# Performance work log

Measured on AMD Instinct MI355X. Metric: run time of the kernel, lower is better.

## Reference

```python
import jax, jax.numpy as jnp
import numpy as np

D_MODEL = 2048
N_EXPERTS = 8
LOSS_SCALE = 3e-06


def setup_inputs() -> dict:
    key = jax.random.key(0)
    k_x, k_wr, k_br, k_w, k_b = jax.random.split(key, 5)
    s = 1.0 / np.sqrt(D_MODEL)
    x = jax.random.normal(k_x, (4, 2048, D_MODEL), dtype=jnp.float32)
    # router: nn.Linear(D, E) -> weight (E, D), bias (E,)
    Wr = jax.random.uniform(k_wr, (N_EXPERTS, D_MODEL), dtype=jnp.float32, minval=-s, maxval=s)
    br = jax.random.uniform(k_br, (N_EXPERTS,), dtype=jnp.float32, minval=-s, maxval=s)
    # experts: E stacked nn.Linear(D, D) -> weight (E, D_out, D_in), bias (E, D)
    W = jax.random.uniform(k_w, (N_EXPERTS, D_MODEL, D_MODEL), dtype=jnp.float32, minval=-s, maxval=s)
    b = jax.random.uniform(k_b, (N_EXPERTS, D_MODEL), dtype=jnp.float32, minval=-s, maxval=s)
    return {"x": x, "Wr": Wr, "br": br, "W": W, "b": b}


def reference(x, Wr, br, W, b):
    B, S, D = x.shape
    E = Wr.shape[0]
    xt = x.reshape(B * S, D)          # (T, D)
    T = xt.shape[0]

    logits = xt @ Wr.T + br           # (T, E)
    probs = jax.nn.softmax(logits, axis=-1)
    idx = jnp.argmax(probs, axis=-1)  # top-1 expert per token
    topp = jnp.max(probs, axis=-1)    # gating weight
    onehot = jax.nn.one_hot(idx, E, dtype=xt.dtype)  # (T, E)

    # auxiliary load-balancing loss (matches torch compute_loss exactly)
    fractions = onehot.mean(axis=0)                              # (E,)
    probability = (onehot * topp[:, None]).sum(axis=0) / (T * T)  # (E,)
    loss = jnp.sum(fractions * probability) * LOSS_SCALE * E

    # all-expert outputs then top-1 select (dense grouped GEMM form)
    y_all = jnp.einsum('td,efd->tef', xt, W) + b[None, :, :]     # (T, E, D)
    y = jnp.einsum('tef,te->tf', y_all, onehot) * topp[:, None]  # (T, D)
    return y.reshape(B, S, D), loss
```

## Files before the change

kernel.cpp:

```cpp
#include <hip/hip_runtime.h>

typedef unsigned short u16;
typedef unsigned int u32;
typedef __attribute__((ext_vector_type(8))) __bf16 bf16x8;
typedef __attribute__((ext_vector_type(4))) float f32x4;

#define T_TOK 8192
#define DMODEL 2048
#define N_EXP 8

__device__ __forceinline__ u32 f2bf_bits(float f) {
    u32 u = __builtin_bit_cast(u32, f);
    return (u + 0x7fffu + ((u >> 16) & 1u)) >> 16;
}
__device__ __forceinline__ u32 pack2(float a, float b) {
    return f2bf_bits(a) | (f2bf_bits(b) << 16);
}

__device__ __forceinline__ void load_lds16(const u16* g, u16* l) {
    void* gnc = (void*)g;
    __builtin_amdgcn_global_load_lds(
        (__attribute__((address_space(1))) void*)gnc,
        (__attribute__((address_space(3))) void*)l,
        16, 0, 0);
}

__global__ void zero_kernel(u32* p) {
    p[threadIdx.x] = 0u;
}

__global__ void __launch_bounds__(256) convert_w_kernel(const float* __restrict__ W,
                                                        u16* __restrict__ Wb) {
    size_t i = ((size_t)blockIdx.x * 256 + threadIdx.x) * 8;
    float4 a = *(const float4*)(W + i);
    float4 b = *(const float4*)(W + i + 4);
    uint4 o;
    o.x = pack2(a.x, a.y);
    o.y = pack2(a.z, a.w);
    o.z = pack2(b.x, b.y);
    o.w = pack2(b.z, b.w);
    *(uint4*)(Wb + i) = o;
}

__global__ void __launch_bounds__(256) router_kernel(const float* __restrict__ x,
                                                     const float* __restrict__ Wr,
                                                     const float* __restrict__ br,
                                                     u16* __restrict__ xb,
                                                     int* __restrict__ perm,
                                                     float* __restrict__ topp,
                                                     int* __restrict__ counts,
                                                     float* __restrict__ sumt) {
    __shared__ int sEid[16];
    __shared__ float sTp[16];

    int tid = threadIdx.x;
    int lane = tid & 63;
    int w = tid >> 6;
    int t0 = blockIdx.x * 16 + w * 4;

    float acc[4][8];
#pragma unroll
    for (int tk = 0; tk < 4; tk++)
#pragma unroll
        for (int e = 0; e < 8; e++) acc[tk][e] = 0.0f;

#pragma unroll
    for (int i = 0; i < 8; i++) {
        int vidx = i * 64 + lane;
        float4 wv[8];
#pragma unroll
        for (int e = 0; e < 8; e++)
            wv[e] = *(const float4*)(Wr + e * DMODEL + vidx * 4);
#pragma unroll
        for (int tk = 0; tk < 4; tk++) {
            int t = t0 + tk;
            float4 xv = ((const float4*)(x + ((size_t)t << 11)))[vidx];
            uint2 pk;
            pk.x = pack2(xv.x, xv.y);
            pk.y = pack2(xv.z, xv.w);
            *(uint2*)(xb + ((size_t)t << 11) + (size_t)vidx * 4) = pk;
#pragma unroll
            for (int e = 0; e < 8; e++) {
                acc[tk][e] = fmaf(xv.x, wv[e].x, fmaf(xv.y, wv[e].y,
                              fmaf(xv.z, wv[e].z, fmaf(xv.w, wv[e].w, acc[tk][e]))));
            }
        }
    }
#pragma unroll
    for (int off = 32; off; off >>= 1)
#pragma unroll
        for (int tk = 0; tk < 4; tk++)
#pragma unroll
            for (int e = 0; e < 8; e++)
                acc[tk][e] += __shfl_xor(acc[tk][e], off, 64);

    if (lane == 0) {
#pragma unroll
        for (int tk = 0; tk < 4; tk++) {
            float lg[8];
#pragma unroll
            for (int e = 0; e < 8; e++) lg[e] = acc[tk][e] + br[e];
            float m = lg[0];
            int am = 0;
#pragma unroll
            for (int e = 1; e < 8; e++)
                if (lg[e] > m) { m = lg[e]; am = e; }
            float s = 0.0f;
#pragma unroll
            for (int e = 0; e < 8; e++) s += __expf(lg[e] - m);
            float tp = 1.0f / s;
            sEid[w * 4 + tk] = am;
            sTp[w * 4 + tk] = tp;
            topp[t0 + tk] = tp;
        }
    }
    __syncthreads();
    if (tid < 16) {
        int e = sEid[tid];
        float tp = sTp[tid];
        int pos = atomicAdd(&counts[e * 16], 1);
        perm[(e << 13) + pos] = blockIdx.x * 16 + tid;
        atomicAdd(&sumt[e * 16], tp);
    }
}

__global__ void __launch_bounds__(256) moe_gemm_kernel(const u16* __restrict__ xb,
                                                       const u16* __restrict__ Wb,
                                                       const float* __restrict__ bias,
                                                       const int* __restrict__ perm,
                                                       const int* __restrict__ counts,
                                                       const float* __restrict__ topp,
                                                       float* __restrict__ out) {
    __shared__ __align__(16) u16 lds[32768];

    int bid = blockIdx.x;
    int e  = bid & 7;
    int tc = (bid >> 3) & 15;
    int tr = bid >> 7;
    int cnt = counts[e * 16];
    int row0 = tr << 7;
    if (row0 >= cnt) return;
    int n0 = tc << 7;

    int tid = threadIdx.x;
    int lane = tid & 63;
    int w = tid >> 6;

    const int* permE = perm + (e << 13);
    const u16* WbE = Wb + ((size_t)e << 22);
    const u16* gA[4];
    const u16* gB[4];
    int sOff[4];
#pragma unroll
    for (int j = 0; j < 4; j++) {
        int s = tid + j * 256;
        int r = s >> 3;
        int cg = (s & 7) ^ (r & 7);
        int ta = permE[min(row0 + r, cnt - 1)];
        gA[j] = xb + ((size_t)ta << 11) + (cg << 3);
        gB[j] = WbE + ((size_t)(n0 + r) << 11) + (cg << 3);
        sOff[j] = s * 8;
    }

    int mbase = (w & 1) << 6;
    int nbase = (w >> 1) << 6;
    int mrow = lane & 15;
    int kq = lane >> 4;
    int s7 = mrow & 7;

    f32x4 acc[4][4];
#pragma unroll
    for (int mi = 0; mi < 4; mi++)
#pragma unroll
        for (int ni = 0; ni < 4; ni++)
            acc[mi][ni] = (f32x4){0.0f, 0.0f, 0.0f, 0.0f};

#pragma unroll
    for (int j = 0; j < 4; j++) load_lds16(gA[j], lds + sOff[j]);
#pragma unroll
    for (int j = 0; j < 4; j++) load_lds16(gB[j], lds + 16384 + sOff[j]);

    for (int kt = 0; kt < 32; kt++) {
        int p = kt & 1;
        if (kt < 31) {
            int ko = (kt + 1) << 6;
            u16* la = lds + (p ^ 1) * 8192;
            u16* lb = lds + 16384 + (p ^ 1) * 8192;
#pragma unroll
            for (int j = 0; j < 4; j++) load_lds16(gA[j] + ko, la + sOff[j]);
#pragma unroll
            for (int j = 0; j < 4; j++) load_lds16(gB[j] + ko, lb + sOff[j]);
            asm volatile("s_waitcnt vmcnt(8)" ::: "memory");
        } else {
            asm volatile("s_waitcnt vmcnt(0)" ::: "memory");
        }
        asm volatile("s_barrier" ::: "memory");

        const u16* bufA = lds + p * 8192;
        const u16* bufB = lds + 16384 + p * 8192;
#pragma unroll
        for (int ks = 0; ks < 2; ks++) {
            int kcs = (ks * 4 + kq) ^ s7;
            int aO = ((mbase + mrow) * 8 + kcs) * 8;
            int bO = ((nbase + mrow) * 8 + kcs) * 8;
            bf16x8 af[4], bf[4];
#pragma unroll
            for (int i = 0; i < 4; i++) {
                af[i] = *(const bf16x8*)(bufA + aO + i * 1024);
                bf[i] = *(const bf16x8*)(bufB + bO + i * 1024);
            }
#pragma unroll
            for (int mi = 0; mi < 4; mi++)
#pragma unroll
                for (int ni = 0; ni < 4; ni++)
                    acc[mi][ni] = __builtin_amdgcn_mfma_f32_16x16x32_bf16(
                        af[mi], bf[ni], acc[mi][ni], 0, 0, 0);
        }
        asm volatile("s_barrier" ::: "memory");
    }

    const float* bE = bias + (e << 11);
    float bv[4];
#pragma unroll
    for (int ni = 0; ni < 4; ni++)
        bv[ni] = bE[n0 + nbase + ni * 16 + (lane & 15)];

    int rb = row0 + mbase + ((lane >> 4) << 2);
#pragma unroll
    for (int mi = 0; mi < 4; mi++) {
        int t_[4]; float tp_[4]; int v_[4];
#pragma unroll
        for (int r = 0; r < 4; r++) {
            int gr = rb + mi * 16 + r;
            v_[r] = gr < cnt;
            int grc = v_[r] ? gr : (cnt - 1);
            t_[r] = permE[grc];
            tp_[r] = topp[t_[r]];
        }
#pragma unroll
        for (int ni = 0; ni < 4; ni++) {
            int col = n0 + nbase + ni * 16 + (lane & 15);
            f32x4 v = acc[mi][ni];
#pragma unroll
            for (int r = 0; r < 4; r++) {
                if (v_[r])
                    out[((size_t)t_[r] << 11) + col] = (v[r] + bv[ni]) * tp_[r];
            }
        }
    }
}

__global__ void loss_kernel(const int* __restrict__ counts,
                            const float* __restrict__ sumt,
                            float* __restrict__ lossOut) {
    if (threadIdx.x == 0) {
        float acc = 0.0f;
        for (int e = 0; e < 8; e++) {
            float frac = (float)counts[e * 16] / 8192.0f;
            float prob = sumt[e * 16] / (8192.0f * 8192.0f);
            acc = fmaf(frac, prob, acc);
        }
        lossOut[0] = acc * 3e-6f * 8.0f;
    }
}

extern "C" void kernel_launch(void* const* d_in, const int* in_sizes, int n_in,
                              void* d_out, int out_size, void* d_ws, size_t ws_size,
                              hipStream_t stream) {
    const float* x  = (const float*)d_in[0];
    const float* Wr = (const float*)d_in[1];
    const float* br = (const float*)d_in[2];
    const float* W  = (const float*)d_in[3];
    const float* b  = (const float*)d_in[4];
    float* out = (float*)d_out;

    char* ws = (char*)d_ws;
    u16* Wb     = (u16*)ws;
    u16* xb     = (u16*)(ws + 67108864);
    int* perm   = (int*)(ws + 100663296);
    float* topp = (float*)(ws + 100925440);
    int* counts = (int*)(ws + 100958208);
    float* sumt = (float*)(ws + 100958720);

    zero_kernel<<<1, 256, 0, stream>>>((u32*)counts);
    convert_w_kernel<<<(8 * 2048 * 2048) / (256 * 8), 256, 0, stream>>>(W, Wb);
    router_kernel<<<T_TOK / 16, 256, 0, stream>>>(x, Wr, br, xb, perm, topp, counts, sumt);
    moe_gemm_kernel<<<N_EXP * 64 * 16, 256, 0, stream>>>(xb, Wb, b, perm, counts, topp, out);
    loss_kernel<<<1, 64, 0, stream>>>(counts, sumt, out + (size_t)T_TOK * DMODEL);
}
```

Baseline: 410.0 us.

## Enlarge MoE GEMM tile to 256x256 with phased prefetch and fuse prep kernels

The grouped GEMM moves from 128x128 tiles with 4 waves to 256x256 tiles with 8 waves. Global-to-LDS loads are interleaved across eight compute phases per two k-steps, with fine-grained waitcnt, extra barriers and setprio around the MFMA bursts. Weight conversion and routing are merged into one launch. The larger tile raises data reuse and lowers operand traffic, at the cost of more registers and LDS per block, more tail waste on partial expert tiles, and fewer blocks overall.

```diff
diff --git a/kernel.cpp b/kernel.cpp
--- a/kernel.cpp
+++ b/kernel.cpp
@@ -8,6 +8,7 @@
 #define T_TOK 8192
 #define DMODEL 2048
 #define N_EXP 8
+#define NT 32
 
 __device__ __forceinline__ u32 f2bf_bits(float f) {
     u32 u = __builtin_bit_cast(u32, f);
@@ -29,34 +30,38 @@
     p[threadIdx.x] = 0u;
 }
 
-__global__ void __launch_bounds__(256) convert_w_kernel(const float* __restrict__ W,
-                                                        u16* __restrict__ Wb) {
-    size_t i = ((size_t)blockIdx.x * 256 + threadIdx.x) * 8;
-    float4 a = *(const float4*)(W + i);
-    float4 b = *(const float4*)(W + i + 4);
-    uint4 o;
-    o.x = pack2(a.x, a.y);
-    o.y = pack2(a.z, a.w);
-    o.z = pack2(b.x, b.y);
-    o.w = pack2(b.z, b.w);
-    *(uint4*)(Wb + i) = o;
-}
-
-__global__ void __launch_bounds__(256) router_kernel(const float* __restrict__ x,
-                                                     const float* __restrict__ Wr,
-                                                     const float* __restrict__ br,
-                                                     u16* __restrict__ xb,
-                                                     int* __restrict__ perm,
-                                                     float* __restrict__ topp,
-                                                     int* __restrict__ counts,
-                                                     float* __restrict__ sumt) {
+__global__ void __launch_bounds__(256) prep_kernel(const float* __restrict__ x,
+                                                   const float* __restrict__ Wr,
+                                                   const float* __restrict__ br,
+                                                   const float* __restrict__ W,
+                                                   u16* __restrict__ Wb,
+                                                   u16* __restrict__ xb,
+                                                   int* __restrict__ perm,
+                                                   float* __restrict__ topp,
+                                                   int* __restrict__ counts,
+                                                   float* __restrict__ sumt) {
     __shared__ int sEid[16];
     __shared__ float sTp[16];
 
+    int bx = blockIdx.x;
     int tid = threadIdx.x;
+
+    if (bx >= 512) {
+        size_t i = ((size_t)(bx - 512) * 256 + tid) * 8;
+        float4 a = *(const float4*)(W + i);
+        float4 c = *(const float4*)(W + i + 4);
+        uint4 o;
+        o.x = pack2(a.x, a.y);
+        o.y = pack2(a.z, a.w);
+        o.z = pack2(c.x, c.y);
+        o.w = pack2(c.z, c.w);
+        *(uint4*)(Wb + i) = o;
+        return;
+    }
+
     int lane = tid & 63;
     int w = tid >> 6;
-    int t0 = blockIdx.x * 16 + w * 4;
+    int t0 = bx * 16 + w * 4;
 
     float acc[4][8];
 #pragma unroll
@@ -119,41 +124,44 @@
         int e = sEid[tid];
         float tp = sTp[tid];
         int pos = atomicAdd(&counts[e * 16], 1);
-        perm[(e << 13) + pos] = blockIdx.x * 16 + tid;
+        perm[(e << 13) + pos] = bx * 16 + tid;
         atomicAdd(&sumt[e * 16], tp);
     }
 }
 
-__global__ void __launch_bounds__(256) moe_gemm_kernel(const u16* __restrict__ xb,
-                                                       const u16* __restrict__ Wb,
-                                                       const float* __restrict__ bias,
-                                                       const int* __restrict__ perm,
-                                                       const int* __restrict__ counts,
-                                                       const float* __restrict__ topp,
-                                                       float* __restrict__ out) {
-    __shared__ __align__(16) u16 lds[32768];
+__global__ void __launch_bounds__(512, 2) moe_gemm_kernel(const u16* __restrict__ xb,
+                                                          const u16* __restrict__ Wb,
+                                                          const float* __restrict__ bias,
+                                                          const int* __restrict__ perm,
+                                                          const int* __restrict__ counts,
+                                                          const float* __restrict__ topp,
+                                                          float* __restrict__ out) {
+    __shared__ __align__(16) u16 lds[65536];
 
     int bid = blockIdx.x;
     int e  = bid & 7;
-    int tc = (bid >> 3) & 15;
-    int tr = bid >> 7;
+    int tc = (bid >> 3) & 7;
+    int tr = bid >> 6;
     int cnt = counts[e * 16];
-    int row0 = tr << 7;
+    int row0 = tr << 8;
     if (row0 >= cnt) return;
-    int n0 = tc << 7;
+    int n0 = tc << 8;
 
     int tid = threadIdx.x;
     int lane = tid & 63;
-    int w = tid >> 6;
+    int wid = tid >> 6;
+    int wr = wid >> 2;
+    int wc = wid & 3;
 
     const int* permE = perm + (e << 13);
     const u16* WbE = Wb + ((size_t)e << 22);
+
     const u16* gA[4];
     const u16* gB[4];
     int sOff[4];
 #pragma unroll
     for (int j = 0; j < 4; j++) {
-        int s = tid + j * 256;
+        int s = tid + j * 512;
         int r = s >> 3;
         int cg = (s & 7) ^ (r & 7);
         int ta = permE[min(row0 + r, cnt - 1)];
@@ -162,72 +170,93 @@
         sOff[j] = s * 8;
     }
 
-    int mbase = (w & 1) << 6;
-    int nbase = (w >> 1) << 6;
+#define STG_A(QB, J, KO) load_lds16(gA[J] + (KO), lds + (QB) + sOff[J])
+#define STG_B(QB, J, KO) load_lds16(gB[J] + (KO), lds + (QB) + 32768 + sOff[J])
+#define VM4 asm volatile("s_waitcnt vmcnt(4)" ::: "memory")
+#define VM2 asm volatile("s_waitcnt vmcnt(2)" ::: "memory")
+#define VMN ((void)0)
+
+    STG_A(0, 0, 0); STG_A(0, 2, 0);
+    STG_B(0, 0, 0); STG_B(0, 1, 0);
+    STG_B(0, 2, 0); STG_B(0, 3, 0);
+    STG_A(0, 1, 0); STG_A(0, 3, 0);
+
     int mrow = lane & 15;
     int kq = lane >> 4;
     int s7 = mrow & 7;
-
-    f32x4 acc[4][4];
-#pragma unroll
-    for (int mi = 0; mi < 4; mi++)
+    int mb = wr << 7;
+    int nb = wc << 6;
+
+    f32x4 acc[8][4];
+#pragma unroll
+    for (int mi = 0; mi < 8; mi++)
 #pragma unroll
         for (int ni = 0; ni < 4; ni++)
             acc[mi][ni] = (f32x4){0.0f, 0.0f, 0.0f, 0.0f};
 
-#pragma unroll
-    for (int j = 0; j < 4; j++) load_lds16(gA[j], lds + sOff[j]);
-#pragma unroll
-    for (int j = 0; j < 4; j++) load_lds16(gB[j], lds + 16384 + sOff[j]);
-
-    for (int kt = 0; kt < 32; kt++) {
-        int p = kt & 1;
-        if (kt < 31) {
-            int ko = (kt + 1) << 6;
-            u16* la = lds + (p ^ 1) * 8192;
-            u16* lb = lds + 16384 + (p ^ 1) * 8192;
-#pragma unroll
-            for (int j = 0; j < 4; j++) load_lds16(gA[j] + ko, la + sOff[j]);
-#pragma unroll
-            for (int j = 0; j < 4; j++) load_lds16(gB[j] + ko, lb + sOff[j]);
-            asm volatile("s_waitcnt vmcnt(8)" ::: "memory");
-        } else {
-            asm volatile("s_waitcnt vmcnt(0)" ::: "memory");
-        }
-        asm volatile("s_barrier" ::: "memory");
-
-        const u16* bufA = lds + p * 8192;
-        const u16* bufB = lds + 16384 + p * 8192;
-#pragma unroll
-        for (int ks = 0; ks < 2; ks++) {
-            int kcs = (ks * 4 + kq) ^ s7;
-            int aO = ((mbase + mrow) * 8 + kcs) * 8;
-            int bO = ((nbase + mrow) * 8 + kcs) * 8;
-            bf16x8 af[4], bf[4];
-#pragma unroll
-            for (int i = 0; i < 4; i++) {
-                af[i] = *(const bf16x8*)(bufA + aO + i * 1024);
-                bf[i] = *(const bf16x8*)(bufB + bO + i * 1024);
-            }
-#pragma unroll
-            for (int mi = 0; mi < 4; mi++)
-#pragma unroll
-                for (int ni = 0; ni < 4; ni++)
-                    acc[mi][ni] = __builtin_amdgcn_mfma_f32_16x16x32_bf16(
-                        af[mi], bf[ni], acc[mi][ni], 0, 0, 0);
-        }
-        asm volatile("s_barrier" ::: "memory");
+    VM2;
+    asm volatile("s_barrier" ::: "memory");
+
+#define PHASE(QB, MG, KS, S1, S2, VMW)                                         \
+    {                                                                          \
+        int kcs = ((KS) * 4 + kq) ^ s7;                                        \
+        const u16* pa = lds + (QB) + ((mb + (MG) * 64 + mrow) * 8 + kcs) * 8;  \
+        const u16* pb = lds + (QB) + 32768 + ((nb + mrow) * 8 + kcs) * 8;      \
+        bf16x8 a0 = *(const bf16x8*)(pa);                                      \
+        bf16x8 a1 = *(const bf16x8*)(pa + 1024);                               \
+        bf16x8 a2 = *(const bf16x8*)(pa + 2048);                               \
+        bf16x8 a3 = *(const bf16x8*)(pa + 3072);                               \
+        bf16x8 b0 = *(const bf16x8*)(pb);                                      \
+        bf16x8 b1 = *(const bf16x8*)(pb + 1024);                               \
+        bf16x8 b2 = *(const bf16x8*)(pb + 2048);                               \
+        bf16x8 b3 = *(const bf16x8*)(pb + 3072);                               \
+        S1; S2;                                                                \
+        asm volatile("s_barrier" ::: "memory");                                \
+        __builtin_amdgcn_s_setprio(1);                                         \
+        acc[(MG)*4+0][0] = __builtin_amdgcn_mfma_f32_16x16x32_bf16(a0, b0, acc[(MG)*4+0][0], 0, 0, 0); \
+        acc[(MG)*4+0][1] = __builtin_amdgcn_mfma_f32_16x16x32_bf16(a0, b1, acc[(MG)*4+0][1], 0, 0, 0); \
+        acc[(MG)*4+0][2] = __builtin_amdgcn_mfma_f32_16x16x32_bf16(a0, b2, acc[(MG)*4+0][2], 0, 0, 0); \
+        acc[(MG)*4+0][3] = __builtin_amdgcn_mfma_f32_16x16x32_bf16(a0, b3, acc[(MG)*4+0][3], 0, 0, 0); \
+        acc[(MG)*4+1][0] = __builtin_amdgcn_mfma_f32_16x16x32_bf16(a1, b0, acc[(MG)*4+1][0], 0, 0, 0); \
+        acc[(MG)*4+1][1] = __builtin_amdgcn_mfma_f32_16x16x32_bf16(a1, b1, acc[(MG)*4+1][1], 0, 0, 0); \
+        acc[(MG)*4+1][2] = __builtin_amdgcn_mfma_f32_16x16x32_bf16(a1, b2, acc[(MG)*4+1][2], 0, 0, 0); \
+        acc[(MG)*4+1][3] = __builtin_amdgcn_mfma_f32_16x16x32_bf16(a1, b3, acc[(MG)*4+1][3], 0, 0, 0); \
+        acc[(MG)*4+2][0] = __builtin_amdgcn_mfma_f32_16x16x32_bf16(a2, b0, acc[(MG)*4+2][0], 0, 0, 0); \
+        acc[(MG)*4+2][1] = __builtin_amdgcn_mfma_f32_16x16x32_bf16(a2, b1, acc[(MG)*4+2][1], 0, 0, 0); \
+        acc[(MG)*4+2][2] = __builtin_amdgcn_mfma_f32_16x16x32_bf16(a2, b2, acc[(MG)*4+2][2], 0, 0, 0); \
+        acc[(MG)*4+2][3] = __builtin_amdgcn_mfma_f32_16x16x32_bf16(a2, b3, acc[(MG)*4+2][3], 0, 0, 0); \
+        acc[(MG)*4+3][0] = __builtin_amdgcn_mfma_f32_16x16x32_bf16(a3, b0, acc[(MG)*4+3][0], 0, 0, 0); \
+        acc[(MG)*4+3][1] = __builtin_amdgcn_mfma_f32_16x16x32_bf16(a3, b1, acc[(MG)*4+3][1], 0, 0, 0); \
+        acc[(MG)*4+3][2] = __builtin_amdgcn_mfma_f32_16x16x32_bf16(a3, b2, acc[(MG)*4+3][2], 0, 0, 0); \
+        acc[(MG)*4+3][3] = __builtin_amdgcn_mfma_f32_16x16x32_bf16(a3, b3, acc[(MG)*4+3][3], 0, 0, 0); \
+        __builtin_amdgcn_s_setprio(0);                                         \
+        VMW;                                                                   \
+        asm volatile("s_barrier" ::: "memory");                                \
+    }
+
+#pragma unroll 1
+    for (int t = 0; t < NT; t += 2) {
+        int ko1 = (t + 1) << 6;
+        int ko2 = (t + 2 < NT ? t + 2 : NT - 1) << 6;
+        PHASE(0,     0, 0, STG_A(16384, 0, ko1), STG_A(16384, 2, ko1), VMN);
+        PHASE(0,     0, 1, STG_B(16384, 0, ko1), STG_B(16384, 1, ko1), VM4);
+        PHASE(0,     1, 0, STG_B(16384, 2, ko1), STG_B(16384, 3, ko1), VMN);
+        PHASE(0,     1, 1, STG_A(16384, 1, ko1), STG_A(16384, 3, ko1), VM2);
+        PHASE(16384, 0, 0, STG_A(0, 0, ko2), STG_A(0, 2, ko2), VMN);
+        PHASE(16384, 0, 1, STG_B(0, 0, ko2), STG_B(0, 1, ko2), VM4);
+        PHASE(16384, 1, 0, STG_B(0, 2, ko2), STG_B(0, 3, ko2), VMN);
+        PHASE(16384, 1, 1, STG_A(0, 1, ko2), STG_A(0, 3, ko2), VM2);
     }
 
     const float* bE = bias + (e << 11);
     float bv[4];
 #pragma unroll
     for (int ni = 0; ni < 4; ni++)
-        bv[ni] = bE[n0 + nbase + ni * 16 + (lane & 15)];
-
-    int rb = row0 + mbase + ((lane >> 4) << 2);
-#pragma unroll
-    for (int mi = 0; mi < 4; mi++) {
+        bv[ni] = bE[n0 + nb + ni * 16 + mrow];
+
+    int rb = row0 + mb + ((lane >> 4) << 2);
+#pragma unroll
+    for (int mi = 0; mi < 8; mi++) {
         int t_[4]; float tp_[4]; int v_[4];
 #pragma unroll
         for (int r = 0; r < 4; r++) {
@@ -239,7 +268,7 @@
         }
 #pragma unroll
         for (int ni = 0; ni < 4; ni++) {
-            int col = n0 + nbase + ni * 16 + (lane & 15);
+            int col = n0 + nb + ni * 16 + mrow;
             f32x4 v = acc[mi][ni];
 #pragma unroll
             for (int r = 0; r < 4; r++) {
@@ -283,8 +312,9 @@
     float* sumt = (float*)(ws + 100958720);
 
     zero_kernel<<<1, 256, 0, stream>>>((u32*)counts);
-    convert_w_kernel<<<(8 * 2048 * 2048) / (256 * 8), 256, 0, stream>>>(W, Wb);
-    router_kernel<<<T_TOK / 16, 256, 0, stream>>>(x, Wr, br, xb, perm, topp, counts, sumt);
-    moe_gemm_kernel<<<N_EXP * 64 * 16, 256, 0, stream>>>(xb, Wb, b, perm, counts, topp, out);
+    prep_kernel<<<512 + 16384, 256, 0, stream>>>(x, Wr, br, W, Wb, xb, perm,
+                                                 topp, counts, sumt);
+    moe_gemm_kernel<<<N_EXP * 8 * 32, 512, 0, stream>>>(xb, Wb, b, perm, counts,
+                                                        topp, out);
     loss_kernel<<<1, 64, 0, stream>>>(counts, sumt, out + (size_t)T_TOK * DMODEL);
 }
```

After: 404.0 us. No clear change (-1.4%).
